# Kernel tuning notes

Hardware: AMD Instinct MI355X
Metric: run time of the kernel (lower is better)

The kernel has to match this reference:

```python
import jax, jax.numpy as jnp
import numpy as np

B, T, N, D = 8, 12, 883, 128
H, C = 8, 16          # heads, out_channels per head (D = H*C, concat=True)
E = 7000              # edges per graph instance
FF = 2048             # feed_forward_dim
NEG_SLOPE = 0.2       # GATv2Conv default negative_slope


def setup_inputs() -> dict:
    key = jax.random.key(0)
    ks = jax.random.split(key, 16)
    s = 0.05
    return {
        "x": jax.random.normal(ks[0], (B, T, N, D), jnp.float32),
        "edge_index": jax.random.randint(ks[1], (2, E), 0, N, dtype=jnp.int64),
        # GATv2Conv params (lin_l, lin_r each have bias by default; att vector; final bias)
        "Wl": jax.random.normal(ks[2], (D, H * C), jnp.float32) * s,
        "bl": jnp.zeros((H * C,), jnp.float32),
        "Wr": jax.random.normal(ks[3], (D, H * C), jnp.float32) * s,
        "br": jnp.zeros((H * C,), jnp.float32),
        "att": jax.random.normal(ks[4], (H, C), jnp.float32) * s,
        "bias_gat": jnp.zeros((H * C,), jnp.float32),
        # FFN
        "W1": jax.random.normal(ks[5], (D, FF), jnp.float32) * s,
        "b1": jnp.zeros((FF,), jnp.float32),
        "W2": jax.random.normal(ks[6], (FF, D), jnp.float32) * s,
        "b2": jnp.zeros((D,), jnp.float32),
        # LayerNorms
        "g1": jnp.ones((D,), jnp.float32),
        "be1": jnp.zeros((D,), jnp.float32),
        "g2": jnp.ones((D,), jnp.float32),
        "be2": jnp.zeros((D,), jnp.float32),
    }


def _layer_norm(x, g, b, eps=1e-5):
    mu = x.mean(-1, keepdims=True)
    var = ((x - mu) ** 2).mean(-1, keepdims=True)
    return (x - mu) * jax.lax.rsqrt(var + eps) * g + b


def _forward(x, edge_index, Wl, bl, Wr, br, att, bias_gat,
             W1, b1, W2, b2, g1, be1, g2, be2):
    B_, T_, N_, D_ = x.shape
    BT = B_ * T_
    TN = BT * N_
    # expand shared edge_index across B*T instances (per torch code)
    offsets = jnp.arange(BT, dtype=edge_index.dtype) * N_
    ee = (edge_index[None, :, :] + offsets[:, None, None]).transpose(1, 0, 2).reshape(2, -1)
    # PyG GATv2Conv default: add self loops
    loops = jnp.arange(TN, dtype=edge_index.dtype)
    src = jnp.concatenate([ee[0], loops])  # message source j
    dst = jnp.concatenate([ee[1], loops])  # message target i

    xf = x.reshape(TN, D_)
    x_l = (xf @ Wl + bl).reshape(TN, H, C)
    x_r = (xf @ Wr + br).reshape(TN, H, C)

    # GATv2 attention: leaky_relu(x_l[j] + x_r[i]) . att
    e = x_l[src] + x_r[dst]                        # [Etot, H, C]
    e = jnp.where(e > 0, e, NEG_SLOPE * e)
    score = jnp.einsum('ehc,hc->eh', e, att)       # [Etot, H]

    # segment softmax over incoming edges per target node
    smax = jax.ops.segment_max(score, dst, num_segments=TN)
    a = jnp.exp(score - smax[dst])
    denom = jax.ops.segment_sum(a, dst, num_segments=TN)
    alpha = a / denom[dst]                          # [Etot, H]

    # scatter-add aggregation of alpha * x_l[src]
    agg = jax.ops.segment_sum(alpha[:, :, None] * x_l[src], dst, num_segments=TN)
    x_gat = (agg.reshape(TN, H * C) + bias_gat).reshape(B_, T_, N_, D_)

    h = _layer_norm(x + x_gat, g1, be1)
    ff = (jnp.maximum(h.reshape(-1, D_) @ W1 + b1, 0.0) @ W2 + b2).reshape(h.shape)
    return _layer_norm(h + ff, g2, be2)


def reference(x, edge_index, Wl, bl, Wr, br, att, bias_gat,
              W1, b1, W2, b2, g1, be1, g2, be2):
    return _forward(x, edge_index, Wl, bl, Wr, br, att, bias_gat,
                    W1, b1, W2, b2, g1, be1, g2, be2)
```

## Files before the change

kernel.cpp:

```cpp
#include <hip/hip_runtime.h>
#include <stdint.h>

typedef unsigned short u16;

#define TN    84768
#define NNODE 883
#define DD    128
#define EE    7000
#define FFDIM 2048

typedef short bf16x8 __attribute__((ext_vector_type(8)));
typedef float f32x4  __attribute__((ext_vector_type(4)));
typedef __attribute__((address_space(3))) u16 lds_u16;
typedef const __attribute__((address_space(1))) u16 glb_u16;

__device__ __forceinline__ float bf2f(u16 u) {
    unsigned int x = ((unsigned int)u) << 16;
    return __uint_as_float(x);
}
__device__ __forceinline__ u16 f2bf(float f) {
    unsigned int x = __float_as_uint(f);
    x += 0x7FFFu + ((x >> 16) & 1u);
    return (u16)(x >> 16);
}
__device__ __forceinline__ u16 cleanu(u16 u) {
    return (((u >> 7) & 0xFF) == 0xFF) ? (u16)0 : u;
}
__device__ __forceinline__ u16 cleanf(float f) {
    unsigned b = __float_as_uint(f);
    if (((b >> 23) & 0xFF) == 0xFF) return 0;
    return cleanu(f2bf(f));
}

__global__ __launch_bounds__(256) void k_detect(const unsigned* __restrict__ x,
                                                int* __restrict__ flag) {
    __shared__ int cnt;
    if (threadIdx.x == 0) cnt = 0;
    __syncthreads();
    unsigned w = x[threadIdx.x];
    unsigned e = (w >> 7) & 0xFF;
    int ok = (e >= 96 && e <= 144) || ((w & 0xFFFFu) == 0);
    atomicAdd(&cnt, ok);
    __syncthreads();
    if (threadIdx.x == 0) flag[0] = (cnt < 200) ? 1 : 0;
}

__global__ __launch_bounds__(256) void k_prep(const void* Wl, const void* Wr,
                                              const void* W1, const void* W2,
                                              const void* bl, const void* br,
                                              const void* att, const void* bgat,
                                              const void* b1, const void* b2,
                                              const void* g1, const void* be1,
                                              const void* g2, const void* be2,
                                              u16* __restrict__ wlrT,
                                              u16* __restrict__ w1T,
                                              u16* __restrict__ w2T,
                                              u16* __restrict__ canon,
                                              const int* __restrict__ flag) {
    int f32 = *flag;
    int i = blockIdx.x * 256 + threadIdx.x;
    if (i < 16384) {
        int r = i >> 7, c = i & 127;
        u16 v = f32 ? cleanf(((const float*)Wl)[i]) : cleanu(((const u16*)Wl)[i]);
        wlrT[c * 128 + r] = v;
    } else if (i < 32768) {
        int idx = i - 16384;
        int r = idx >> 7, c = idx & 127;
        u16 v = f32 ? cleanf(((const float*)Wr)[idx]) : cleanu(((const u16*)Wr)[idx]);
        wlrT[16384 + c * 128 + r] = v;
    } else if (i < 294912) {
        int idx = i - 32768;
        int r = idx >> 11, c = idx & 2047;
        u16 v = f32 ? cleanf(((const float*)W1)[idx]) : cleanu(((const u16*)W1)[idx]);
        w1T[c * 128 + r] = v;
    } else if (i < 557056) {
        int idx = i - 294912;
        int r = idx >> 7, c = idx & 127;
        u16 v = f32 ? cleanf(((const float*)W2)[idx]) : cleanu(((const u16*)W2)[idx]);
        w2T[c * 2048 + r] = v;
    } else if (i < 560256) {
        int p = i - 557056;
        const void* src; int off;
        if      (p < 128)  { src = bl;   off = 0; }
        else if (p < 256)  { src = br;   off = 128; }
        else if (p < 384)  { src = att;  off = 256; }
        else if (p < 512)  { src = bgat; off = 384; }
        else if (p < 2560) { src = b1;   off = 512; }
        else if (p < 2688) { src = b2;   off = 2560; }
        else if (p < 2816) { src = g1;   off = 2688; }
        else if (p < 2944) { src = be1;  off = 2816; }
        else if (p < 3072) { src = g2;   off = 2944; }
        else               { src = be2;  off = 3072; }
        int j = p - off;
        canon[p] = f32 ? cleanf(((const float*)src)[j]) : cleanu(((const u16*)src)[j]);
    }
}

__global__ __launch_bounds__(1024) void k_csr(const int* __restrict__ ew,
                                              int* __restrict__ row_off,
                                              int* __restrict__ col) {
    __shared__ int cnt[NNODE];
    __shared__ int offs[NNODE + 1];
    __shared__ int cur[NNODE];
    __shared__ int flag;
    int tid = threadIdx.x;
    if (tid == 0) flag = 0;
    for (int i = tid; i < NNODE; i += 1024) cnt[i] = 0;
    __syncthreads();
    int f = 0;
    for (int j = tid; j < EE; j += 1024) f |= ew[2 * j + 1];
    if (f) atomicOr(&flag, 1);
    __syncthreads();
    bool is32 = (flag != 0);
    for (int e = tid; e < EE; e += 1024) {
        int dst = is32 ? ew[EE + e] : ew[2 * EE + 2 * e];
        if ((unsigned)dst < NNODE) atomicAdd(&cnt[dst], 1);
    }
    __syncthreads();
    if (tid == 0) {
        int run = 0;
        for (int i = 0; i < NNODE; ++i) { offs[i] = run; run += cnt[i]; }
        offs[NNODE] = run;
    }
    __syncthreads();
    for (int i = tid; i < NNODE; i += 1024) cur[i] = offs[i];
    __syncthreads();
    for (int e = tid; e < EE; e += 1024) {
        int src = is32 ? ew[e] : ew[2 * e];
        int dst = is32 ? ew[EE + e] : ew[2 * EE + 2 * e];
        if ((unsigned)dst < NNODE && (unsigned)src < NNODE) {
            int p = atomicAdd(&cur[dst], 1);
            if (p < EE) col[p] = src;
        }
    }
    __syncthreads();
    for (int i = tid; i <= NNODE; i += 1024) row_off[i] = offs[i];
}

__global__ __launch_bounds__(256) void k_linlr(const void* __restrict__ xraw,
                                               const u16* __restrict__ wlrT,
                                               const u16* __restrict__ canon,
                                               u16* __restrict__ xl, u16* __restrict__ xr,
                                               const int* __restrict__ flag) {
    __shared__ __align__(16) u16 a_tile[64 * 136];
    int f32 = *flag;
    int tid = threadIdx.x;
    int m0 = blockIdx.x * 64;
    for (int it = 0; it < 4; ++it) {
        int idx = it * 256 + tid;
        int row = idx >> 4, cc = idx & 15;
        int gm = m0 + row;
        u16 tmp[8];
#pragma unroll
        for (int j = 0; j < 8; ++j) tmp[j] = 0;
        if (gm < TN) {
            size_t base = (size_t)gm * DD + cc * 8;
            if (f32) {
                float4 v0 = *(const float4*)((const float*)xraw + base);
                float4 v1 = *(const float4*)((const float*)xraw + base + 4);
                tmp[0] = cleanf(v0.x); tmp[1] = cleanf(v0.y);
                tmp[2] = cleanf(v0.z); tmp[3] = cleanf(v0.w);
                tmp[4] = cleanf(v1.x); tmp[5] = cleanf(v1.y);
                tmp[6] = cleanf(v1.z); tmp[7] = cleanf(v1.w);
            } else {
                uint4 v = *(const uint4*)((const u16*)xraw + base);
                unsigned wv[4] = {v.x, v.y, v.z, v.w};
#pragma unroll
                for (int j = 0; j < 8; ++j)
                    tmp[j] = cleanu((u16)((wv[j >> 1] >> ((j & 1) * 16)) & 0xFFFFu));
            }
        }
        uint4 o;
        o.x = (unsigned)tmp[0] | ((unsigned)tmp[1] << 16);
        o.y = (unsigned)tmp[2] | ((unsigned)tmp[3] << 16);
        o.z = (unsigned)tmp[4] | ((unsigned)tmp[5] << 16);
        o.w = (unsigned)tmp[6] | ((unsigned)tmp[7] << 16);
        *(uint4*)(a_tile + row * 136 + cc * 8) = o;
    }
    __syncthreads();
    int wave = tid >> 6, lane = tid & 63, n16 = lane & 15, q = lane >> 4;
    f32x4 acc[16];
#pragma unroll
    for (int t = 0; t < 16; ++t) acc[t] = (f32x4){0, 0, 0, 0};
    const u16* arow = a_tile + (16 * wave + n16) * 136;
#pragma unroll
    for (int ks = 0; ks < 4; ++ks) {
        bf16x8 a = *(const bf16x8*)(arow + ks * 32 + q * 8);
#pragma unroll
        for (int t = 0; t < 16; ++t) {
            bf16x8 b = *(const bf16x8*)(wlrT + ((size_t)(t * 16 + n16)) * DD + ks * 32 + q * 8);
            acc[t] = __builtin_amdgcn_mfma_f32_16x16x32_bf16(a, b, acc[t], 0, 0, 0);
        }
    }
#pragma unroll
    for (int t = 0; t < 16; ++t) {
        int cc = (t & 7) * 16 + n16;
        float bias = bf2f(canon[(t < 8 ? 0 : 128) + cc]);
        u16* dst = (t < 8 ? xl : xr);
#pragma unroll
        for (int reg = 0; reg < 4; ++reg) {
            int mrow = m0 + 16 * wave + 4 * q + reg;
            if (mrow < TN) dst[(size_t)mrow * DD + cc] = f2bf(acc[t][reg] + bias);
        }
    }
}

__device__ __forceinline__ float segsum16(float p) {
    p += __shfl_xor(p, 1, 16);
    p += __shfl_xor(p, 2, 16);
    p += __shfl_xor(p, 4, 16);
    p += __shfl_xor(p, 8, 16);
    return p;
}

__global__ __launch_bounds__(256) void k_gat(const void* __restrict__ xraw,
                                             const u16* __restrict__ xl,
                                             const u16* xr,
                                             const u16* __restrict__ canon,
                                             const int* __restrict__ row_off,
                                             const int* __restrict__ col,
                                             u16* h1,
                                             const int* __restrict__ flag) {
    int f32 = *flag;
    int tid = threadIdx.x;
    int wave = tid >> 6, lane = tid & 63;
    int g = blockIdx.x * 4 + wave;
    int bt = g / NNODE;
    int i = g - bt * NNODE;
    size_t gbase = (size_t)g * DD;
    const u16* xlrow0 = xl + (size_t)bt * NNODE * DD;
    int c2 = lane * 2;
    unsigned uxr = *(const unsigned*)(xr + gbase + c2);
    float xr0 = __uint_as_float(uxr << 16);
    float xr1 = __uint_as_float(uxr & 0xFFFF0000u);
    unsigned uat = *(const unsigned*)(canon + 256 + c2);
    float at0 = __uint_as_float(uat << 16);
    float at1 = __uint_as_float(uat & 0xFFFF0000u);
    unsigned uxs = *(const unsigned*)(xl + gbase + c2);
    float xs0 = __uint_as_float(uxs << 16);
    float xs1 = __uint_as_float(uxs & 0xFFFF0000u);
    float t0 = xs0 + xr0, t1 = xs1 + xr1;
    t0 = fmaxf(t0, 0.2f * t0); t1 = fmaxf(t1, 0.2f * t1);
    float p = t0 * at0 + t1 * at1;
    p += __shfl_xor(p, 1, 8);
    p += __shfl_xor(p, 2, 8);
    p += __shfl_xor(p, 4, 8);
    p = fminf(fmaxf(p, -30.f), 30.f);
    float w = __expf(p);
    float denom = w;
    float a0 = w * xs0, a1 = w * xs1;
    int r0 = row_off[i], r1 = row_off[i + 1];
    for (int e = r0; e < r1; ++e) {
        int j = __builtin_amdgcn_readfirstlane(col[e]);
        if ((unsigned)j >= NNODE) continue;
        unsigned uj = *(const unsigned*)(xlrow0 + (size_t)j * DD + c2);
        float x0 = __uint_as_float(uj << 16);
        float x1 = __uint_as_float(uj & 0xFFFF0000u);
        float u0 = x0 + xr0, u1 = x1 + xr1;
        u0 = fmaxf(u0, 0.2f * u0); u1 = fmaxf(u1, 0.2f * u1);
        float q = u0 * at0 + u1 * at1;
        q += __shfl_xor(q, 1, 8);
        q += __shfl_xor(q, 2, 8);
        q += __shfl_xor(q, 4, 8);
        q = fminf(fmaxf(q, -30.f), 30.f);
        float ww = __expf(q);
        denom += ww;
        a0 += ww * x0;
        a1 += ww * x1;
    }
    float inv = 1.f / denom;
    unsigned ubg = *(const unsigned*)(canon + 384 + c2);
    float res0, res1;
    if (f32) {
        float2 rr = *(const float2*)((const float*)xraw + gbase + c2);
        unsigned b0 = __float_as_uint(rr.x), b1 = __float_as_uint(rr.y);
        res0 = (((b0 >> 23) & 0xFF) == 0xFF) ? 0.f : rr.x;
        res1 = (((b1 >> 23) & 0xFF) == 0xFF) ? 0.f : rr.y;
    } else {
        unsigned ux = *(const unsigned*)((const u16*)xraw + gbase + c2);
        res0 = bf2f(cleanu((u16)(ux & 0xFFFFu)));
        res1 = bf2f(cleanu((u16)(ux >> 16)));
    }
    float pre0 = a0 * inv + __uint_as_float(ubg << 16) + res0;
    float pre1 = a1 * inv + __uint_as_float(ubg & 0xFFFF0000u) + res1;
    float sum = pre0 + pre1, sq = pre0 * pre0 + pre1 * pre1;
    for (int off = 32; off; off >>= 1) {
        sum += __shfl_xor(sum, off);
        sq  += __shfl_xor(sq, off);
    }
    float mu = sum * (1.0f / 128.0f);
    float var = fmaxf(sq * (1.0f / 128.0f) - mu * mu, 0.f);
    float rs = rsqrtf(var + 1e-5f);
    unsigned ug = *(const unsigned*)(canon + 2688 + c2);
    unsigned ub = *(const unsigned*)(canon + 2816 + c2);
    float h0 = (pre0 - mu) * rs * __uint_as_float(ug << 16) + __uint_as_float(ub << 16);
    float h1v = (pre1 - mu) * rs * __uint_as_float(ug & 0xFFFF0000u) + __uint_as_float(ub & 0xFFFF0000u);
    unsigned out = (unsigned)f2bf(h0) | ((unsigned)f2bf(h1v) << 16);
    *(unsigned*)(h1 + gbase + c2) = out;
}

__global__ __launch_bounds__(256, 3) void k_ffn(const u16* __restrict__ h1,
                                                const u16* __restrict__ w1T,
                                                const u16* __restrict__ w2T,
                                                const u16* __restrict__ canon,
                                                void* __restrict__ outraw,
                                                const int* __restrict__ flag) {
    __shared__ __align__(16) u16 w1b[64 * 128];
    __shared__ __align__(16) u16 w2b[128 * 64];
    __shared__ __align__(16) u16 s_t[128 * 72];
    int f32 = *flag;
    int tid = threadIdx.x;
    int wave = tid >> 6, lane = tid & 63, n16 = lane & 15, q = lane >> 4;
    int m0 = blockIdx.x * 128;
    int swz = n16 & 7;
    bf16x8 af[2][4];
#pragma unroll
    for (int sub = 0; sub < 2; ++sub) {
        int gm = m0 + 32 * wave + 16 * sub + n16;
#pragma unroll
        for (int ks = 0; ks < 4; ++ks) {
            if (gm < TN) {
                uint4 v = *(const uint4*)(h1 + (size_t)gm * DD + ks * 32 + q * 8);
                af[sub][ks] = *(const bf16x8*)&v;
            } else {
                uint4 z = make_uint4(0, 0, 0, 0);
                af[sub][ks] = *(const bf16x8*)&z;
            }
        }
    }
    f32x4 acc2[2][8];
#pragma unroll
    for (int sub = 0; sub < 2; ++sub)
#pragma unroll
        for (int t = 0; t < 8; ++t) acc2[sub][t] = (f32x4){0, 0, 0, 0};
    int w1r[4], w1b_log[4];
#pragma unroll
    for (int i = 0; i < 4; ++i) {
        w1r[i] = 16 * wave + 4 * i + (lane >> 4);
        w1b_log[i] = (lane & 15) ^ (w1r[i] & 7);
    }
    int w2r[4], w2b_log[4];
#pragma unroll
    for (int i = 0; i < 4; ++i) {
        w2r[i] = 32 * wave + 8 * i + (lane >> 3);
        w2b_log[i] = (lane & 7) ^ (w2r[i] & 7);
    }
    u16* srow_w0 = s_t + (32 * wave + 4 * q) * 72;
    u16* srow_w1 = s_t + (32 * wave + 16 + 4 * q) * 72;
    const u16* srow_r0 = s_t + (32 * wave + n16) * 72;
    const u16* srow_r1 = s_t + (32 * wave + 16 + n16) * 72;
    for (int ch = 0; ch < 32; ++ch) {
        int f0 = ch * 64;
        __syncthreads();
#pragma unroll
        for (int i = 0; i < 4; ++i) {
            glb_u16* g1 = (glb_u16*)(w1T + (size_t)(f0 + w1r[i]) * DD + w1b_log[i] * 8);
            lds_u16* l1 = (lds_u16*)(w1b + (16 * wave + 4 * i) * 128);
            __builtin_amdgcn_global_load_lds((const __attribute__((address_space(1))) unsigned*)g1,
                                             (__attribute__((address_space(3))) unsigned*)l1,
                                             16, 0, 0);
        }
#pragma unroll
        for (int i = 0; i < 4; ++i) {
            glb_u16* g2 = (glb_u16*)(w2T + (size_t)w2r[i] * FFDIM + f0 + w2b_log[i] * 8);
            lds_u16* l2 = (lds_u16*)(w2b + (32 * wave + 8 * i) * 64);
            __builtin_amdgcn_global_load_lds((const __attribute__((address_space(1))) unsigned*)g2,
                                             (__attribute__((address_space(3))) unsigned*)l2,
                                             16, 0, 0);
        }
        __syncthreads();
#pragma unroll
        for (int t = 0; t < 4; ++t) {
            f32x4 a10 = (f32x4){0, 0, 0, 0};
            f32x4 a11 = (f32x4){0, 0, 0, 0};
#pragma unroll
            for (int ks = 0; ks < 4; ++ks) {
                bf16x8 b = *(const bf16x8*)(w1b + (t * 16 + n16) * 128 + (((ks * 4 + q) ^ swz) * 8));
                a10 = __builtin_amdgcn_mfma_f32_16x16x32_bf16(af[0][ks], b, a10, 0, 0, 0);
                a11 = __builtin_amdgcn_mfma_f32_16x16x32_bf16(af[1][ks], b, a11, 0, 0, 0);
            }
            float bb = bf2f(canon[512 + f0 + t * 16 + n16]);
#pragma unroll
            for (int reg = 0; reg < 4; ++reg) {
                float v0 = a10[reg] + bb;
                float v1 = a11[reg] + bb;
                v0 = v0 > 0.f ? v0 : 0.f;
                v1 = v1 > 0.f ? v1 : 0.f;
                srow_w0[reg * 72 + t * 16 + n16] = f2bf(v0);
                srow_w1[reg * 72 + t * 16 + n16] = f2bf(v1);
            }
        }
        asm volatile("" ::: "memory");
#pragma unroll
        for (int ks2 = 0; ks2 < 2; ++ks2) {
            bf16x8 a20 = *(const bf16x8*)(srow_r0 + ks2 * 32 + q * 8);
            bf16x8 a21 = *(const bf16x8*)(srow_r1 + ks2 * 32 + q * 8);
#pragma unroll
            for (int t = 0; t < 8; ++t) {
                bf16x8 b = *(const bf16x8*)(w2b + (t * 16 + n16) * 64 + (((ks2 * 4 + q) ^ swz) * 8));
                acc2[0][t] = __builtin_amdgcn_mfma_f32_16x16x32_bf16(a20, b, acc2[0][t], 0, 0, 0);
                acc2[1][t] = __builtin_amdgcn_mfma_f32_16x16x32_bf16(a21, b, acc2[1][t], 0, 0, 0);
            }
        }
        asm volatile("" ::: "memory");
    }
    float b2v[8], g2v[8], e2v[8];
#pragma unroll
    for (int t = 0; t < 8; ++t) {
        int col = t * 16 + n16;
        b2v[t] = bf2f(canon[2560 + col]);
        g2v[t] = bf2f(canon[2944 + col]);
        e2v[t] = bf2f(canon[3072 + col]);
    }
#pragma unroll
    for (int sub = 0; sub < 2; ++sub) {
#pragma unroll
        for (int reg = 0; reg < 4; ++reg) {
            int row = 32 * wave + 16 * sub + 4 * q + reg;
            int gm = m0 + row;
            bool ok = gm < TN;
            size_t gb = (size_t)(ok ? gm : 0) * DD;
            float v[8]; float s1 = 0.f, s2 = 0.f;
#pragma unroll
            for (int t = 0; t < 8; ++t) {
                float hres = bf2f(h1[gb + t * 16 + n16]);
                v[t] = acc2[sub][t][reg] + b2v[t] + hres;
                s1 += v[t]; s2 += v[t] * v[t];
            }
            s1 = segsum16(s1);
            s2 = segsum16(s2);
            float mu = s1 * (1.f / 128.f);
            float var = fmaxf(s2 * (1.f / 128.f) - mu * mu, 0.f);
            float rs = rsqrtf(var + 1e-5f);
            if (ok) {
#pragma unroll
                for (int t = 0; t < 8; ++t) {
                    float r = (v[t] - mu) * rs * g2v[t] + e2v[t];
                    if (f32) ((float*)outraw)[gb + t * 16 + n16] = r;
                    else     ((u16*)outraw)[gb + t * 16 + n16] = f2bf(r);
                }
            }
        }
    }
}

extern "C" void kernel_launch(void* const* d_in, const int* in_sizes, int n_in,
                              void* d_out, int out_size, void* d_ws, size_t ws_size,
                              hipStream_t stream) {
    const void* x    = d_in[0];
    const int* eidx  = (const int*)d_in[1];
    const void* Wl   = d_in[2];
    const void* bl   = d_in[3];
    const void* Wr   = d_in[4];
    const void* br   = d_in[5];
    const void* att  = d_in[6];
    const void* bgat = d_in[7];
    const void* W1   = d_in[8];
    const void* b1   = d_in[9];
    const void* W2   = d_in[10];
    const void* b2   = d_in[11];
    const void* g1   = d_in[12];
    const void* be1  = d_in[13];
    const void* g2   = d_in[14];
    const void* be2  = d_in[15];

    char* ws = (char*)d_ws;
    int* flag   = (int*)(ws);
    int* rowoff = (int*)(ws + 4096);
    int* colw   = (int*)(ws + 8192);
    u16* canon  = (u16*)(ws + 36864);
    u16* wlrT   = (u16*)(ws + 65536);
    u16* w1T    = (u16*)(ws + 131072);
    u16* w2T    = (u16*)(ws + 655360);
    u16* xl     = (u16*)(ws + 1179648);
    u16* xr     = (u16*)(ws + 22880256);
    u16* h1     = xr;

    k_csr<<<1, 1024, 0, stream>>>(eidx, rowoff, colw);
    k_detect<<<1, 256, 0, stream>>>((const unsigned*)x, flag);
    k_prep<<<2189, 256, 0, stream>>>(Wl, Wr, W1, W2, bl, br, att, bgat, b1, b2,
                                     g1, be1, g2, be2, wlrT, w1T, w2T, canon, flag);
    k_linlr<<<(TN + 63) / 64, 256, 0, stream>>>(x, wlrT, canon, xl, xr, flag);
    k_gat<<<TN / 4, 256, 0, stream>>>(x, xl, xr, canon, rowoff, colw, h1, flag);
    k_ffn<<<(TN + 127) / 128, 256, 0, stream>>>(h1, w1T, w2T, canon, d_out, flag);
}
```

Before: 400.0 us.

## Retile FFN waves as a 2x2 M/N grid and unroll GAT edge loop by two

The FFN kernel now arranges its four waves as a 2x2 grid, each covering 64 rows and half of the columns. Each weight fragment read from LDS therefore feeds four MFMAs instead of two, which cuts LDS B-operand traffic, at the cost of an extra block barrier per chunk and a cross-wave LayerNorm reduction through LDS. The GAT aggregation loop handles two edges per iteration to overlap the gathers and shuffles. Invalid-source edges are now filtered when building the CSR, so the per-edge bounds check can be dropped.

```diff
diff --git a/kernel.cpp b/kernel.cpp
--- a/kernel.cpp
+++ b/kernel.cpp
@@ -113,8 +113,9 @@
     __syncthreads();
     bool is32 = (flag != 0);
     for (int e = tid; e < EE; e += 1024) {
+        int src = is32 ? ew[e] : ew[2 * e];
         int dst = is32 ? ew[EE + e] : ew[2 * EE + 2 * e];
-        if ((unsigned)dst < NNODE) atomicAdd(&cnt[dst], 1);
+        if ((unsigned)dst < NNODE && (unsigned)src < NNODE) atomicAdd(&cnt[dst], 1);
     }
     __syncthreads();
     if (tid == 0) {
@@ -250,9 +251,33 @@
     float denom = w;
     float a0 = w * xs0, a1 = w * xs1;
     int r0 = row_off[i], r1 = row_off[i + 1];
-    for (int e = r0; e < r1; ++e) {
+    int e = r0;
+    for (; e + 1 < r1; e += 2) {
+        int j0 = __builtin_amdgcn_readfirstlane(col[e]);
+        int j1 = __builtin_amdgcn_readfirstlane(col[e + 1]);
+        unsigned ua = *(const unsigned*)(xlrow0 + (size_t)j0 * DD + c2);
+        unsigned ub = *(const unsigned*)(xlrow0 + (size_t)j1 * DD + c2);
+        float xa0 = __uint_as_float(ua << 16), xa1 = __uint_as_float(ua & 0xFFFF0000u);
+        float xb0 = __uint_as_float(ub << 16), xb1 = __uint_as_float(ub & 0xFFFF0000u);
+        float ua0 = xa0 + xr0, ua1 = xa1 + xr1;
+        float ub0 = xb0 + xr0, ub1 = xb1 + xr1;
+        ua0 = fmaxf(ua0, 0.2f * ua0); ua1 = fmaxf(ua1, 0.2f * ua1);
+        ub0 = fmaxf(ub0, 0.2f * ub0); ub1 = fmaxf(ub1, 0.2f * ub1);
+        float qa = ua0 * at0 + ua1 * at1;
+        float qb = ub0 * at0 + ub1 * at1;
+        qa += __shfl_xor(qa, 1, 8); qb += __shfl_xor(qb, 1, 8);
+        qa += __shfl_xor(qa, 2, 8); qb += __shfl_xor(qb, 2, 8);
+        qa += __shfl_xor(qa, 4, 8); qb += __shfl_xor(qb, 4, 8);
+        qa = fminf(fmaxf(qa, -30.f), 30.f);
+        qb = fminf(fmaxf(qb, -30.f), 30.f);
+        float wa = __expf(qa);
+        float wb = __expf(qb);
+        denom += wa + wb;
+        a0 += wa * xa0 + wb * xb0;
+        a1 += wa * xa1 + wb * xb1;
+    }
+    if (e < r1) {
         int j = __builtin_amdgcn_readfirstlane(col[e]);
-        if ((unsigned)j >= NNODE) continue;
         unsigned uj = *(const unsigned*)(xlrow0 + (size_t)j * DD + c2);
         float x0 = __uint_as_float(uj << 16);
         float x1 = __uint_as_float(uj & 0xFFFF0000u);
@@ -292,9 +317,9 @@
     float var = fmaxf(sq * (1.0f / 128.0f) - mu * mu, 0.f);
     float rs = rsqrtf(var + 1e-5f);
     unsigned ug = *(const unsigned*)(canon + 2688 + c2);
-    unsigned ub = *(const unsigned*)(canon + 2816 + c2);
-    float h0 = (pre0 - mu) * rs * __uint_as_float(ug << 16) + __uint_as_float(ub << 16);
-    float h1v = (pre1 - mu) * rs * __uint_as_float(ug & 0xFFFF0000u) + __uint_as_float(ub & 0xFFFF0000u);
+    unsigned ub2 = *(const unsigned*)(canon + 2816 + c2);
+    float h0 = (pre0 - mu) * rs * __uint_as_float(ug << 16) + __uint_as_float(ub2 << 16);
+    float h1v = (pre1 - mu) * rs * __uint_as_float(ug & 0xFFFF0000u) + __uint_as_float(ub2 & 0xFFFF0000u);
     unsigned out = (unsigned)f2bf(h0) | ((unsigned)f2bf(h1v) << 16);
     *(unsigned*)(h1 + gbase + c2) = out;
 }
@@ -311,12 +336,13 @@
     int f32 = *flag;
     int tid = threadIdx.x;
     int wave = tid >> 6, lane = tid & 63, n16 = lane & 15, q = lane >> 4;
+    int mi = wave >> 1, ni = wave & 1;
     int m0 = blockIdx.x * 128;
     int swz = n16 & 7;
-    bf16x8 af[2][4];
-#pragma unroll
-    for (int sub = 0; sub < 2; ++sub) {
-        int gm = m0 + 32 * wave + 16 * sub + n16;
+    bf16x8 af[4][4];
+#pragma unroll
+    for (int sub = 0; sub < 4; ++sub) {
+        int gm = m0 + 64 * mi + 16 * sub + n16;
 #pragma unroll
         for (int ks = 0; ks < 4; ++ks) {
             if (gm < TN) {
@@ -328,11 +354,11 @@
             }
         }
     }
-    f32x4 acc2[2][8];
-#pragma unroll
-    for (int sub = 0; sub < 2; ++sub)
-#pragma unroll
-        for (int t = 0; t < 8; ++t) acc2[sub][t] = (f32x4){0, 0, 0, 0};
+    f32x4 acc2[4][4];
+#pragma unroll
+    for (int sub = 0; sub < 4; ++sub)
+#pragma unroll
+        for (int t = 0; t < 4; ++t) acc2[sub][t] = (f32x4){0, 0, 0, 0};
     int w1r[4], w1b_log[4];
 #pragma unroll
     for (int i = 0; i < 4; ++i) {
@@ -345,10 +371,6 @@
         w2r[i] = 32 * wave + 8 * i + (lane >> 3);
         w2b_log[i] = (lane & 7) ^ (w2r[i] & 7);
     }
-    u16* srow_w0 = s_t + (32 * wave + 4 * q) * 72;
-    u16* srow_w1 = s_t + (32 * wave + 16 + 4 * q) * 72;
-    const u16* srow_r0 = s_t + (32 * wave + n16) * 72;
-    const u16* srow_r1 = s_t + (32 * wave + 16 + n16) * 72;
     for (int ch = 0; ch < 32; ++ch) {
         int f0 = ch * 64;
         __syncthreads();
@@ -370,78 +392,100 @@
         }
         __syncthreads();
 #pragma unroll
-        for (int t = 0; t < 4; ++t) {
-            f32x4 a10 = (f32x4){0, 0, 0, 0};
-            f32x4 a11 = (f32x4){0, 0, 0, 0};
+        for (int t = 0; t < 2; ++t) {
+            int cb = 32 * ni + t * 16;
+            f32x4 a1[4];
+#pragma unroll
+            for (int sub = 0; sub < 4; ++sub) a1[sub] = (f32x4){0, 0, 0, 0};
 #pragma unroll
             for (int ks = 0; ks < 4; ++ks) {
-                bf16x8 b = *(const bf16x8*)(w1b + (t * 16 + n16) * 128 + (((ks * 4 + q) ^ swz) * 8));
-                a10 = __builtin_amdgcn_mfma_f32_16x16x32_bf16(af[0][ks], b, a10, 0, 0, 0);
-                a11 = __builtin_amdgcn_mfma_f32_16x16x32_bf16(af[1][ks], b, a11, 0, 0, 0);
-            }
-            float bb = bf2f(canon[512 + f0 + t * 16 + n16]);
-#pragma unroll
-            for (int reg = 0; reg < 4; ++reg) {
-                float v0 = a10[reg] + bb;
-                float v1 = a11[reg] + bb;
-                v0 = v0 > 0.f ? v0 : 0.f;
-                v1 = v1 > 0.f ? v1 : 0.f;
-                srow_w0[reg * 72 + t * 16 + n16] = f2bf(v0);
-                srow_w1[reg * 72 + t * 16 + n16] = f2bf(v1);
-            }
-        }
-        asm volatile("" ::: "memory");
+                bf16x8 b = *(const bf16x8*)(w1b + (cb + n16) * 128 + (((ks * 4 + q) ^ swz) * 8));
+#pragma unroll
+                for (int sub = 0; sub < 4; ++sub)
+                    a1[sub] = __builtin_amdgcn_mfma_f32_16x16x32_bf16(af[sub][ks], b, a1[sub], 0, 0, 0);
+            }
+            float bb = bf2f(canon[512 + f0 + cb + n16]);
+#pragma unroll
+            for (int sub = 0; sub < 4; ++sub)
+#pragma unroll
+                for (int reg = 0; reg < 4; ++reg) {
+                    float v = a1[sub][reg] + bb;
+                    v = v > 0.f ? v : 0.f;
+                    s_t[(64 * mi + 16 * sub + 4 * q + reg) * 72 + cb + n16] = f2bf(v);
+                }
+        }
+        __syncthreads();
 #pragma unroll
         for (int ks2 = 0; ks2 < 2; ++ks2) {
-            bf16x8 a20 = *(const bf16x8*)(srow_r0 + ks2 * 32 + q * 8);
-            bf16x8 a21 = *(const bf16x8*)(srow_r1 + ks2 * 32 + q * 8);
-#pragma unroll
-            for (int t = 0; t < 8; ++t) {
-                bf16x8 b = *(const bf16x8*)(w2b + (t * 16 + n16) * 64 + (((ks2 * 4 + q) ^ swz) * 8));
-                acc2[0][t] = __builtin_amdgcn_mfma_f32_16x16x32_bf16(a20, b, acc2[0][t], 0, 0, 0);
-                acc2[1][t] = __builtin_amdgcn_mfma_f32_16x16x32_bf16(a21, b, acc2[1][t], 0, 0, 0);
-            }
-        }
-        asm volatile("" ::: "memory");
-    }
-    float b2v[8], g2v[8], e2v[8];
-#pragma unroll
-    for (int t = 0; t < 8; ++t) {
-        int col = t * 16 + n16;
+            bf16x8 a2[4];
+#pragma unroll
+            for (int sub = 0; sub < 4; ++sub)
+                a2[sub] = *(const bf16x8*)(s_t + (64 * mi + 16 * sub + n16) * 72 + ks2 * 32 + q * 8);
+#pragma unroll
+            for (int t = 0; t < 4; ++t) {
+                bf16x8 b = *(const bf16x8*)(w2b + (64 * ni + t * 16 + n16) * 64 + (((ks2 * 4 + q) ^ swz) * 8));
+#pragma unroll
+                for (int sub = 0; sub < 4; ++sub)
+                    acc2[sub][t] = __builtin_amdgcn_mfma_f32_16x16x32_bf16(a2[sub], b, acc2[sub][t], 0, 0, 0);
+            }
+        }
+    }
+    __syncthreads();
+    float* red = (float*)w1b;
+    float b2v[4], g2v[4], e2v[4];
+#pragma unroll
+    for (int t = 0; t < 4; ++t) {
+        int col = 64 * ni + t * 16 + n16;
         b2v[t] = bf2f(canon[2560 + col]);
         g2v[t] = bf2f(canon[2944 + col]);
         e2v[t] = bf2f(canon[3072 + col]);
     }
 #pragma unroll
-    for (int sub = 0; sub < 2; ++sub) {
+    for (int sub = 0; sub < 4; ++sub)
 #pragma unroll
         for (int reg = 0; reg < 4; ++reg) {
-            int row = 32 * wave + 16 * sub + 4 * q + reg;
+            int row = 64 * mi + 16 * sub + 4 * q + reg;
+            int gm = m0 + row;
+            size_t gb = (size_t)(gm < TN ? gm : 0) * DD;
+            float s1 = 0.f, s2 = 0.f;
+#pragma unroll
+            for (int t = 0; t < 4; ++t) {
+                float hres = bf2f(h1[gb + 64 * ni + t * 16 + n16]);
+                float v = acc2[sub][t][reg] + b2v[t] + hres;
+                acc2[sub][t][reg] = v;
+                s1 += v; s2 += v * v;
+            }
+            s1 = segsum16(s1);
+            s2 = segsum16(s2);
+            if (n16 == 0) {
+                red[row * 4 + ni * 2]     = s1;
+                red[row * 4 + ni * 2 + 1] = s2;
+            }
+        }
+    __syncthreads();
+#pragma unroll
+    for (int sub = 0; sub < 4; ++sub)
+#pragma unroll
+        for (int reg = 0; reg < 4; ++reg) {
+            int row = 64 * mi + 16 * sub + 4 * q + reg;
             int gm = m0 + row;
             bool ok = gm < TN;
             size_t gb = (size_t)(ok ? gm : 0) * DD;
-            float v[8]; float s1 = 0.f, s2 = 0.f;
-#pragma unroll
-            for (int t = 0; t < 8; ++t) {
-                float hres = bf2f(h1[gb + t * 16 + n16]);
-                v[t] = acc2[sub][t][reg] + b2v[t] + hres;
-                s1 += v[t]; s2 += v[t] * v[t];
-            }
-            s1 = segsum16(s1);
-            s2 = segsum16(s2);
-            float mu = s1 * (1.f / 128.f);
-            float var = fmaxf(s2 * (1.f / 128.f) - mu * mu, 0.f);
+            float ts = red[row * 4] + red[row * 4 + 2];
+            float tq = red[row * 4 + 1] + red[row * 4 + 3];
+            float mu = ts * (1.f / 128.f);
+            float var = fmaxf(tq * (1.f / 128.f) - mu * mu, 0.f);
             float rs = rsqrtf(var + 1e-5f);
             if (ok) {
 #pragma unroll
-                for (int t = 0; t < 8; ++t) {
-                    float r = (v[t] - mu) * rs * g2v[t] + e2v[t];
-                    if (f32) ((float*)outraw)[gb + t * 16 + n16] = r;
-                    else     ((u16*)outraw)[gb + t * 16 + n16] = f2bf(r);
+                for (int t = 0; t < 4; ++t) {
+                    float r = (acc2[sub][t][reg] - mu) * rs * g2v[t] + e2v[t];
+                    size_t oi = gb + 64 * ni + t * 16 + n16;
+                    if (f32) ((float*)outraw)[oi] = r;
+                    else     ((u16*)outraw)[oi] = f2bf(r);
                 }
             }
         }
-    }
 }
 
 extern "C" void kernel_launch(void* const* d_in, const int* in_sizes, int n_in,
```

New measurement: 452.2 us. 13.1% more time.
